# Optimization experiments

Hardware: AMD Instinct MI355X
Metric: run time of the kernel (lower is better)

## Reference

```python
import jax, jax.numpy as jnp
import numpy as np

NUM_CLASSES = 4
IGNORE_INDEX = 0
DELTA_POS = 0.9
DELTA_NEG = 0.1
LAMBDA_ALIGN = 1.0
LAMBDA_SEP = 1.0
EPS = 1e-6
MIN_PIXELS = 1
NORM_EPS = 1e-12  # torch F.normalize default


def setup_inputs() -> dict:
    key = jax.random.key(0)
    k1, k2, k3 = jax.random.split(key, 3)
    B, M, C, D, H, W = 2, 4, 64, 48, 48, 48
    feats = jax.random.normal(k1, (B, M, C, D, H, W), dtype=jnp.float32)
    weights = jax.random.uniform(k2, (B, M, D, H, W), dtype=jnp.float32)
    target = jax.random.randint(k3, (B, 1, D, H, W), 0, NUM_CLASSES, dtype=jnp.int64)
    return {"feats": feats, "weights": weights, "target": target}


def _loss(feats, weights, target):
    B, M, C, D, H, W = feats.shape
    V = D * H * W
    K = NUM_CLASSES
    f = feats.reshape(B, M, C, V)
    w = weights.reshape(B, M, V)
    tgt = target.reshape(B, V)

    # per-class masks [B, K, V]
    onehot = (tgt[:, None, :] == jnp.arange(K)[None, :, None]).astype(f.dtype)
    count = onehot.sum(-1)  # [B, K] pixel counts (independent of m)

    # total weighted mass per (b, m, k) and omega weighting
    tw = jnp.einsum('bmv,bkv->bmk', w, onehot) + EPS          # [B, M, K]
    omega = tw / (count[:, None, :] + EPS)                     # [B, M, K]

    # weighted class means -> prototypes [B, M, K, C]
    num = jnp.einsum('bmcv,bmv,bkv->bmkc', f, w, onehot)
    proto = num / tw[..., None]
    sumsq = jnp.sum(proto * proto, axis=-1)
    norm = jnp.sqrt(jnp.maximum(sumsq, NORM_EPS * NORM_EPS))   # safe sqrt
    proto = proto / jnp.maximum(norm, NORM_EPS)[..., None]

    # validity: enough pixels and not the ignored class
    valid = (count >= MIN_PIXELS) & (jnp.arange(K) != IGNORE_INDEX)[None, :]
    valid = jnp.broadcast_to(valid[:, None, :], (B, M, K))     # [B, M, K]

    # --- align: same class k, modality pairs m < n ---
    sim_a = jnp.einsum('bmkc,bnkc->bmnk', proto, proto)        # [B, M, M, K]
    tri_m = jnp.triu(jnp.ones((M, M), bool), 1)[None, :, :, None]
    pair_a = valid[:, :, None, :] & valid[:, None, :, :] & tri_m
    om_pair = omega[:, :, None, :] * omega[:, None, :, :]
    align_sum = jnp.where(pair_a, om_pair * jax.nn.relu(DELTA_POS - sim_a), 0.0).sum()
    cnt_align = pair_a.sum().astype(f.dtype)

    # --- sep: same modality m, class pairs k1 < k2 ---
    sim_s = jnp.einsum('bmkc,bmlc->bmkl', proto, proto)        # [B, M, K, K]
    tri_k = jnp.triu(jnp.ones((K, K), bool), 1)[None, None, :, :]
    pair_s = valid[:, :, :, None] & valid[:, :, None, :] & tri_k
    sep_sum = jnp.where(pair_s, jax.nn.relu(sim_s - DELTA_NEG), 0.0).sum()
    cnt_sep = pair_s.sum().astype(f.dtype)

    loss_align = align_sum / (cnt_align + EPS)
    loss_sep = sep_sum / (cnt_sep + EPS)
    return LAMBDA_ALIGN * loss_align + LAMBDA_SEP * loss_sep


def reference(feats, weights, target):
    return _loss(feats, weights, target)
```

## Files before the change

### kernel.cpp

```cpp
#include <hip/hip_runtime.h>
#include <math.h>

#define B_ 2
#define M_ 4
#define C_ 64
#define V_ 110592
#define K_ 4
#define EPS_ 1e-6f

#define WS_NUM 0
#define WS_TW  2048
#define WS_CNT 2080
#define WS_TOTAL 2088

__constant__ int PM_[6] = {0,0,0,1,1,2};
__constant__ int PN_[6] = {1,2,3,2,3,3};

__global__ __launch_bounds__(256) void stats_kernel(
    const float* __restrict__ w, const int* __restrict__ tgt,
    float* __restrict__ ws)
{
    const int SA = 27;
    int bm = blockIdx.x / SA;
    int s  = blockIdx.x % SA;
    int b  = bm >> 2;

    const int vec_per = V_ / 4;
    const int chunk   = vec_per / SA;

    const float4* w4 = (const float4*)(w + (size_t)bm * V_);
    const int4*   t4 = (const int4*)(tgt + (size_t)b * V_);

    float tw0=0.f, tw1=0.f, tw2=0.f, tw3=0.f;
    int   c0=0, c1=0, c2=0, c3=0;

    int end = (s + 1) * chunk;
    for (int i = s * chunk + threadIdx.x; i < end; i += 256) {
        float4 wv = w4[i];
        int4   kv = t4[i];
        tw0 += (kv.x==0?wv.x:0.f) + (kv.y==0?wv.y:0.f) + (kv.z==0?wv.z:0.f) + (kv.w==0?wv.w:0.f);
        tw1 += (kv.x==1?wv.x:0.f) + (kv.y==1?wv.y:0.f) + (kv.z==1?wv.z:0.f) + (kv.w==1?wv.w:0.f);
        tw2 += (kv.x==2?wv.x:0.f) + (kv.y==2?wv.y:0.f) + (kv.z==2?wv.z:0.f) + (kv.w==2?wv.w:0.f);
        tw3 += (kv.x==3?wv.x:0.f) + (kv.y==3?wv.y:0.f) + (kv.z==3?wv.z:0.f) + (kv.w==3?wv.w:0.f);
        c0 += (kv.x==0) + (kv.y==0) + (kv.z==0) + (kv.w==0);
        c1 += (kv.x==1) + (kv.y==1) + (kv.z==1) + (kv.w==1);
        c2 += (kv.x==2) + (kv.y==2) + (kv.z==2) + (kv.w==2);
        c3 += (kv.x==3) + (kv.y==3) + (kv.z==3) + (kv.w==3);
    }

    for (int off = 32; off; off >>= 1) {
        tw0 += __shfl_down(tw0, off); tw1 += __shfl_down(tw1, off);
        tw2 += __shfl_down(tw2, off); tw3 += __shfl_down(tw3, off);
        c0  += __shfl_down(c0,  off); c1  += __shfl_down(c1,  off);
        c2  += __shfl_down(c2,  off); c3  += __shfl_down(c3,  off);
    }
    __shared__ float s_tw[4][4];
    __shared__ int   s_c[4][4];
    int wid = threadIdx.x >> 6, lane = threadIdx.x & 63;
    if (lane == 0) {
        s_tw[wid][0]=tw0; s_tw[wid][1]=tw1; s_tw[wid][2]=tw2; s_tw[wid][3]=tw3;
        s_c[wid][0]=c0;   s_c[wid][1]=c1;   s_c[wid][2]=c2;   s_c[wid][3]=c3;
    }
    __syncthreads();
    if (threadIdx.x < 4) {
        int k = threadIdx.x;
        float t = s_tw[0][k] + s_tw[1][k] + s_tw[2][k] + s_tw[3][k];
        atomicAdd(&ws[WS_TW + bm*4 + k], t);
        if ((bm & 3) == 0) {
            int cc = s_c[0][k] + s_c[1][k] + s_c[2][k] + s_c[3][k];
            atomicAdd(&ws[WS_CNT + b*4 + k], (float)cc);
        }
    }
}

__global__ __launch_bounds__(256) void num_kernel(
    const float* __restrict__ f, const float* __restrict__ w,
    const int* __restrict__ tgt, float* __restrict__ ws)
{
    const int S = 4;
    int idx = blockIdx.x;
    int s  = idx & 3;
    int c  = (idx >> 2) & 63;
    int bm = idx >> 8;
    int b  = bm >> 2;

    const int vec_per = V_ / 4;
    const int chunk   = vec_per / S;

    const float4* f4 = (const float4*)(f + ((size_t)bm * C_ + c) * V_);
    const float4* w4 = (const float4*)(w + (size_t)bm * V_);
    const int4*   t4 = (const int4*)(tgt + (size_t)b * V_);

    float a0=0.f, a1=0.f, a2=0.f, a3=0.f;
    int end = (s + 1) * chunk;
    for (int i = s * chunk + threadIdx.x; i < end; i += 256) {
        float4 fv = f4[i];
        float4 wv = w4[i];
        int4   kv = t4[i];
        float p0 = fv.x * wv.x;
        float p1 = fv.y * wv.y;
        float p2 = fv.z * wv.z;
        float p3 = fv.w * wv.w;
        a0 += (kv.x==0?p0:0.f) + (kv.y==0?p1:0.f) + (kv.z==0?p2:0.f) + (kv.w==0?p3:0.f);
        a1 += (kv.x==1?p0:0.f) + (kv.y==1?p1:0.f) + (kv.z==1?p2:0.f) + (kv.w==1?p3:0.f);
        a2 += (kv.x==2?p0:0.f) + (kv.y==2?p1:0.f) + (kv.z==2?p2:0.f) + (kv.w==2?p3:0.f);
        a3 += (kv.x==3?p0:0.f) + (kv.y==3?p1:0.f) + (kv.z==3?p2:0.f) + (kv.w==3?p3:0.f);
    }

    for (int off = 32; off; off >>= 1) {
        a0 += __shfl_down(a0, off); a1 += __shfl_down(a1, off);
        a2 += __shfl_down(a2, off); a3 += __shfl_down(a3, off);
    }
    __shared__ float s_red[4][4];
    int wid = threadIdx.x >> 6, lane = threadIdx.x & 63;
    if (lane == 0) {
        s_red[wid][0]=a0; s_red[wid][1]=a1; s_red[wid][2]=a2; s_red[wid][3]=a3;
    }
    __syncthreads();
    if (threadIdx.x < 4) {
        int k = threadIdx.x;
        float v = s_red[0][k] + s_red[1][k] + s_red[2][k] + s_red[3][k];
        atomicAdd(&ws[WS_NUM + (bm*4 + k)*C_ + c], v);
    }
}

__global__ __launch_bounds__(256) void finalize_kernel(
    const float* __restrict__ ws, float* __restrict__ out)
{
    const float* num = ws + WS_NUM;
    const float* tw  = ws + WS_TW;
    const float* cnt = ws + WS_CNT;

    __shared__ float sp[2048];
    __shared__ float s_scale[32];
    __shared__ float s_om[32];
    __shared__ int   s_valid[32];

    int tid = threadIdx.x;

    for (int i = tid; i < 2048; i += 256) {
        int p = i >> 6;
        sp[i] = num[i] / (tw[p] + EPS_);
    }
    __syncthreads();

    if (tid < 32) {
        float ss = 0.f;
        for (int c = 0; c < 64; ++c) { float v = sp[tid*64 + c]; ss += v*v; }
        float norm = sqrtf(fmaxf(ss, 1e-24f));
        s_scale[tid] = 1.0f / fmaxf(norm, 1e-12f);
        int b = tid >> 4;
        int k = tid & 3;
        float cc = cnt[b*4 + k];
        s_om[tid] = (tw[tid] + EPS_) / (cc + EPS_);
        s_valid[tid] = (cc >= 1.0f) && (k != 0);
    }
    __syncthreads();
    for (int i = tid; i < 2048; i += 256) sp[i] *= s_scale[i >> 6];
    __syncthreads();

    float aS = 0.f, aC = 0.f, sS = 0.f, sC = 0.f;

    if (tid < 48) {
        int b = tid / 24, r = tid % 24;
        int pr = r >> 2, k = r & 3;
        int p1 = (b*4 + PM_[pr])*4 + k;
        int p2 = (b*4 + PN_[pr])*4 + k;
        if (s_valid[p1] && s_valid[p2]) {
            float d = 0.f;
            for (int c = 0; c < 64; ++c) d += sp[p1*64 + c] * sp[p2*64 + c];
            aS = s_om[p1] * s_om[p2] * fmaxf(0.9f - d, 0.f);
            aC = 1.f;
        }
    } else if (tid >= 64 && tid < 112) {
        int t = tid - 64;
        int b = t / 24, r = t % 24;
        int m = r / 6, pr = r % 6;
        int bm = b*4 + m;
        int p1 = bm*4 + PM_[pr];
        int p2 = bm*4 + PN_[pr];
        if (s_valid[p1] && s_valid[p2]) {
            float d = 0.f;
            for (int c = 0; c < 64; ++c) d += sp[p1*64 + c] * sp[p2*64 + c];
            sS = fmaxf(d - 0.1f, 0.f);
            sC = 1.f;
        }
    }

    for (int off = 32; off; off >>= 1) {
        aS += __shfl_down(aS, off); aC += __shfl_down(aC, off);
        sS += __shfl_down(sS, off); sC += __shfl_down(sC, off);
    }
    __shared__ float red[4][4];
    int wid = tid >> 6, lane = tid & 63;
    if (lane == 0) { red[wid][0]=aS; red[wid][1]=aC; red[wid][2]=sS; red[wid][3]=sC; }
    __syncthreads();
    if (tid == 0) {
        float AS=0.f, AC=0.f, SS=0.f, SC=0.f;
        for (int i = 0; i < 4; ++i) { AS+=red[i][0]; AC+=red[i][1]; SS+=red[i][2]; SC+=red[i][3]; }
        out[0] = AS / (AC + EPS_) + SS / (SC + EPS_);
    }
}

extern "C" void kernel_launch(void* const* d_in, const int* in_sizes, int n_in,
                              void* d_out, int out_size, void* d_ws, size_t ws_size,
                              hipStream_t stream)
{
    const float* feats   = (const float*)d_in[0];
    const float* weights = (const float*)d_in[1];
    const int*   target  = (const int*)d_in[2];
    float* out = (float*)d_out;
    float* ws  = (float*)d_ws;

    hipMemsetAsync(d_ws, 0, WS_TOTAL * sizeof(float), stream);
    stats_kernel<<<B_*M_*27, 256, 0, stream>>>(weights, target, ws);
    num_kernel<<<B_*M_*C_*4, 256, 0, stream>>>(feats, weights, target, ws);
    finalize_kernel<<<1, 256, 0, stream>>>(ws, out);
}
```

Baseline: 327.0 us.

## Fuse stats into feature reduction, process two channels per block, drop atomics

Merges the separate weight/count statistics kernel into the main feature-reduction kernel, computed only by channel-0 blocks. Each block now handles two channels so the weight and target loads are shared. Feature loads become nontemporal. Per-split partial sums go to distinct workspace slots that the finalize kernel adds up, which removes the memset and the atomics. The cost is more registers per thread, fewer blocks, and a little extra reduction work in the single-block finalize.

```diff
diff --git a/kernel.cpp b/kernel.cpp
--- a/kernel.cpp
+++ b/kernel.cpp
@@ -5,154 +5,151 @@
 #define M_ 4
 #define C_ 64
 #define V_ 110592
-#define K_ 4
 #define EPS_ 1e-6f
 
-#define WS_NUM 0
-#define WS_TW  2048
-#define WS_CNT 2080
-#define WS_TOTAL 2088
+#define P_NUM 0
+#define P_TW  8192
+#define P_CNT 8320
 
 __constant__ int PM_[6] = {0,0,0,1,1,2};
 __constant__ int PN_[6] = {1,2,3,2,3,3};
 
-__global__ __launch_bounds__(256) void stats_kernel(
-    const float* __restrict__ w, const int* __restrict__ tgt,
-    float* __restrict__ ws)
-{
-    const int SA = 27;
-    int bm = blockIdx.x / SA;
-    int s  = blockIdx.x % SA;
-    int b  = bm >> 2;
-
-    const int vec_per = V_ / 4;
-    const int chunk   = vec_per / SA;
-
-    const float4* w4 = (const float4*)(w + (size_t)bm * V_);
-    const int4*   t4 = (const int4*)(tgt + (size_t)b * V_);
-
-    float tw0=0.f, tw1=0.f, tw2=0.f, tw3=0.f;
-    int   c0=0, c1=0, c2=0, c3=0;
-
-    int end = (s + 1) * chunk;
-    for (int i = s * chunk + threadIdx.x; i < end; i += 256) {
-        float4 wv = w4[i];
-        int4   kv = t4[i];
-        tw0 += (kv.x==0?wv.x:0.f) + (kv.y==0?wv.y:0.f) + (kv.z==0?wv.z:0.f) + (kv.w==0?wv.w:0.f);
-        tw1 += (kv.x==1?wv.x:0.f) + (kv.y==1?wv.y:0.f) + (kv.z==1?wv.z:0.f) + (kv.w==1?wv.w:0.f);
-        tw2 += (kv.x==2?wv.x:0.f) + (kv.y==2?wv.y:0.f) + (kv.z==2?wv.z:0.f) + (kv.w==2?wv.w:0.f);
-        tw3 += (kv.x==3?wv.x:0.f) + (kv.y==3?wv.y:0.f) + (kv.z==3?wv.z:0.f) + (kv.w==3?wv.w:0.f);
-        c0 += (kv.x==0) + (kv.y==0) + (kv.z==0) + (kv.w==0);
-        c1 += (kv.x==1) + (kv.y==1) + (kv.z==1) + (kv.w==1);
-        c2 += (kv.x==2) + (kv.y==2) + (kv.z==2) + (kv.w==2);
-        c3 += (kv.x==3) + (kv.y==3) + (kv.z==3) + (kv.w==3);
-    }
-
-    for (int off = 32; off; off >>= 1) {
-        tw0 += __shfl_down(tw0, off); tw1 += __shfl_down(tw1, off);
-        tw2 += __shfl_down(tw2, off); tw3 += __shfl_down(tw3, off);
-        c0  += __shfl_down(c0,  off); c1  += __shfl_down(c1,  off);
-        c2  += __shfl_down(c2,  off); c3  += __shfl_down(c3,  off);
-    }
-    __shared__ float s_tw[4][4];
-    __shared__ int   s_c[4][4];
-    int wid = threadIdx.x >> 6, lane = threadIdx.x & 63;
-    if (lane == 0) {
-        s_tw[wid][0]=tw0; s_tw[wid][1]=tw1; s_tw[wid][2]=tw2; s_tw[wid][3]=tw3;
-        s_c[wid][0]=c0;   s_c[wid][1]=c1;   s_c[wid][2]=c2;   s_c[wid][3]=c3;
-    }
-    __syncthreads();
-    if (threadIdx.x < 4) {
-        int k = threadIdx.x;
-        float t = s_tw[0][k] + s_tw[1][k] + s_tw[2][k] + s_tw[3][k];
-        atomicAdd(&ws[WS_TW + bm*4 + k], t);
-        if ((bm & 3) == 0) {
-            int cc = s_c[0][k] + s_c[1][k] + s_c[2][k] + s_c[3][k];
-            atomicAdd(&ws[WS_CNT + b*4 + k], (float)cc);
-        }
-    }
-}
-
-__global__ __launch_bounds__(256) void num_kernel(
+typedef float  fvec4 __attribute__((ext_vector_type(4)));
+
+__global__ __launch_bounds__(256) void main_kernel(
     const float* __restrict__ f, const float* __restrict__ w,
     const int* __restrict__ tgt, float* __restrict__ ws)
 {
-    const int S = 4;
     int idx = blockIdx.x;
     int s  = idx & 3;
-    int c  = (idx >> 2) & 63;
-    int bm = idx >> 8;
+    int ch = (idx >> 2) & 31;
+    int bm = idx >> 7;
     int b  = bm >> 2;
-
-    const int vec_per = V_ / 4;
-    const int chunk   = vec_per / S;
-
-    const float4* f4 = (const float4*)(f + ((size_t)bm * C_ + c) * V_);
+    const bool do_stats = (ch == 0);
+
+    const int chunk = (V_ / 4) / 4;
+
+    const fvec4* fa = (const fvec4*)(f + ((size_t)bm * C_ + ch) * V_);
+    const fvec4* fb = (const fvec4*)(f + ((size_t)bm * C_ + ch + 32) * V_);
     const float4* w4 = (const float4*)(w + (size_t)bm * V_);
     const int4*   t4 = (const int4*)(tgt + (size_t)b * V_);
 
-    float a0=0.f, a1=0.f, a2=0.f, a3=0.f;
-    int end = (s + 1) * chunk;
-    for (int i = s * chunk + threadIdx.x; i < end; i += 256) {
-        float4 fv = f4[i];
+    float A[8] = {0,0,0,0,0,0,0,0};
+    float tw[4] = {0,0,0,0};
+    int   cn[4] = {0,0,0,0};
+
+    int beg = s * chunk, end = beg + chunk;
+    for (int i = beg + (int)threadIdx.x; i < end; i += 256) {
+        fvec4  va = __builtin_nontemporal_load(&fa[i]);
+        fvec4  vb = __builtin_nontemporal_load(&fb[i]);
         float4 wv = w4[i];
         int4   kv = t4[i];
-        float p0 = fv.x * wv.x;
-        float p1 = fv.y * wv.y;
-        float p2 = fv.z * wv.z;
-        float p3 = fv.w * wv.w;
-        a0 += (kv.x==0?p0:0.f) + (kv.y==0?p1:0.f) + (kv.z==0?p2:0.f) + (kv.w==0?p3:0.f);
-        a1 += (kv.x==1?p0:0.f) + (kv.y==1?p1:0.f) + (kv.z==1?p2:0.f) + (kv.w==1?p3:0.f);
-        a2 += (kv.x==2?p0:0.f) + (kv.y==2?p1:0.f) + (kv.z==2?p2:0.f) + (kv.w==2?p3:0.f);
-        a3 += (kv.x==3?p0:0.f) + (kv.y==3?p1:0.f) + (kv.z==3?p2:0.f) + (kv.w==3?p3:0.f);
-    }
-
+        float pa0 = va.x * wv.x, pa1 = va.y * wv.y, pa2 = va.z * wv.z, pa3 = va.w * wv.w;
+        float pb0 = vb.x * wv.x, pb1 = vb.y * wv.y, pb2 = vb.z * wv.z, pb3 = vb.w * wv.w;
+        #pragma unroll
+        for (int k = 0; k < 4; ++k) {
+            A[k]     += (kv.x==k?pa0:0.f) + (kv.y==k?pa1:0.f) + (kv.z==k?pa2:0.f) + (kv.w==k?pa3:0.f);
+            A[4 + k] += (kv.x==k?pb0:0.f) + (kv.y==k?pb1:0.f) + (kv.z==k?pb2:0.f) + (kv.w==k?pb3:0.f);
+        }
+        if (do_stats) {
+            #pragma unroll
+            for (int k = 0; k < 4; ++k) {
+                tw[k] += (kv.x==k?wv.x:0.f) + (kv.y==k?wv.y:0.f) + (kv.z==k?wv.z:0.f) + (kv.w==k?wv.w:0.f);
+                cn[k] += (kv.x==k) + (kv.y==k) + (kv.z==k) + (kv.w==k);
+            }
+        }
+    }
+
+    #pragma unroll
     for (int off = 32; off; off >>= 1) {
-        a0 += __shfl_down(a0, off); a1 += __shfl_down(a1, off);
-        a2 += __shfl_down(a2, off); a3 += __shfl_down(a3, off);
-    }
-    __shared__ float s_red[4][4];
+        #pragma unroll
+        for (int j = 0; j < 8; ++j) A[j] += __shfl_down(A[j], off);
+        if (do_stats) {
+            #pragma unroll
+            for (int k = 0; k < 4; ++k) {
+                tw[k] += __shfl_down(tw[k], off);
+                cn[k] += __shfl_down(cn[k], off);
+            }
+        }
+    }
+
+    __shared__ float sA[4][8];
+    __shared__ float sT[4][4];
+    __shared__ int   sC[4][4];
     int wid = threadIdx.x >> 6, lane = threadIdx.x & 63;
     if (lane == 0) {
-        s_red[wid][0]=a0; s_red[wid][1]=a1; s_red[wid][2]=a2; s_red[wid][3]=a3;
-    }
-    __syncthreads();
-    if (threadIdx.x < 4) {
+        #pragma unroll
+        for (int j = 0; j < 8; ++j) sA[wid][j] = A[j];
+        if (do_stats) {
+            #pragma unroll
+            for (int k = 0; k < 4; ++k) { sT[wid][k] = tw[k]; sC[wid][k] = cn[k]; }
+        }
+    }
+    __syncthreads();
+
+    if (threadIdx.x < 8) {
+        int j = threadIdx.x;
+        int k = j & 3;
+        int c = ch + (j >> 2) * 32;
+        float v = sA[0][j] + sA[1][j] + sA[2][j] + sA[3][j];
+        ws[P_NUM + ((bm * C_ + c) * 4 + s) * 4 + k] = v;
+    }
+    if (do_stats && threadIdx.x < 4) {
         int k = threadIdx.x;
-        float v = s_red[0][k] + s_red[1][k] + s_red[2][k] + s_red[3][k];
-        atomicAdd(&ws[WS_NUM + (bm*4 + k)*C_ + c], v);
+        float t = sT[0][k] + sT[1][k] + sT[2][k] + sT[3][k];
+        ws[P_TW + (bm * 4 + s) * 4 + k] = t;
+        if ((bm & 3) == 0) {
+            int cc = sC[0][k] + sC[1][k] + sC[2][k] + sC[3][k];
+            ws[P_CNT + (b * 4 + s) * 4 + k] = (float)cc;
+        }
     }
 }
 
 __global__ __launch_bounds__(256) void finalize_kernel(
     const float* __restrict__ ws, float* __restrict__ out)
 {
-    const float* num = ws + WS_NUM;
-    const float* tw  = ws + WS_TW;
-    const float* cnt = ws + WS_CNT;
-
     __shared__ float sp[2048];
+    __shared__ float s_tw[32];
+    __shared__ float s_cnt[8];
     __shared__ float s_scale[32];
     __shared__ float s_om[32];
     __shared__ int   s_valid[32];
 
     int tid = threadIdx.x;
 
+    if (tid < 32) {
+        int bm = tid >> 2, k = tid & 3;
+        float t = 0.f;
+        #pragma unroll
+        for (int s = 0; s < 4; ++s) t += ws[P_TW + (bm * 4 + s) * 4 + k];
+        s_tw[tid] = t;
+    } else if (tid < 40) {
+        int u = tid - 32, b = u >> 2, k = u & 3;
+        float t = 0.f;
+        #pragma unroll
+        for (int s = 0; s < 4; ++s) t += ws[P_CNT + (b * 4 + s) * 4 + k];
+        s_cnt[u] = t;
+    }
+    __syncthreads();
+
     for (int i = tid; i < 2048; i += 256) {
-        int p = i >> 6;
-        sp[i] = num[i] / (tw[p] + EPS_);
+        int p = i >> 6, c = i & 63;
+        int bm = p >> 2, k = p & 3;
+        float t = 0.f;
+        #pragma unroll
+        for (int s = 0; s < 4; ++s) t += ws[P_NUM + ((bm * C_ + c) * 4 + s) * 4 + k];
+        sp[i] = t / (s_tw[p] + EPS_);
     }
     __syncthreads();
 
     if (tid < 32) {
         float ss = 0.f;
-        for (int c = 0; c < 64; ++c) { float v = sp[tid*64 + c]; ss += v*v; }
+        for (int c = 0; c < 64; ++c) { float v = sp[tid * 64 + c]; ss += v * v; }
         float norm = sqrtf(fmaxf(ss, 1e-24f));
         s_scale[tid] = 1.0f / fmaxf(norm, 1e-12f);
-        int b = tid >> 4;
-        int k = tid & 3;
-        float cc = cnt[b*4 + k];
-        s_om[tid] = (tw[tid] + EPS_) / (cc + EPS_);
+        int b = tid >> 4, k = tid & 3;
+        float cc = s_cnt[b * 4 + k];
+        s_om[tid] = (s_tw[tid] + EPS_) / (cc + EPS_);
         s_valid[tid] = (cc >= 1.0f) && (k != 0);
     }
     __syncthreads();
@@ -164,11 +161,11 @@
     if (tid < 48) {
         int b = tid / 24, r = tid % 24;
         int pr = r >> 2, k = r & 3;
-        int p1 = (b*4 + PM_[pr])*4 + k;
-        int p2 = (b*4 + PN_[pr])*4 + k;
+        int p1 = (b * 4 + PM_[pr]) * 4 + k;
+        int p2 = (b * 4 + PN_[pr]) * 4 + k;
         if (s_valid[p1] && s_valid[p2]) {
             float d = 0.f;
-            for (int c = 0; c < 64; ++c) d += sp[p1*64 + c] * sp[p2*64 + c];
+            for (int c = 0; c < 64; ++c) d += sp[p1 * 64 + c] * sp[p2 * 64 + c];
             aS = s_om[p1] * s_om[p2] * fmaxf(0.9f - d, 0.f);
             aC = 1.f;
         }
@@ -176,17 +173,18 @@
         int t = tid - 64;
         int b = t / 24, r = t % 24;
         int m = r / 6, pr = r % 6;
-        int bm = b*4 + m;
-        int p1 = bm*4 + PM_[pr];
-        int p2 = bm*4 + PN_[pr];
+        int bm = b * 4 + m;
+        int p1 = bm * 4 + PM_[pr];
+        int p2 = bm * 4 + PN_[pr];
         if (s_valid[p1] && s_valid[p2]) {
             float d = 0.f;
-            for (int c = 0; c < 64; ++c) d += sp[p1*64 + c] * sp[p2*64 + c];
+            for (int c = 0; c < 64; ++c) d += sp[p1 * 64 + c] * sp[p2 * 64 + c];
             sS = fmaxf(d - 0.1f, 0.f);
             sC = 1.f;
         }
     }
 
+    #pragma unroll
     for (int off = 32; off; off >>= 1) {
         aS += __shfl_down(aS, off); aC += __shfl_down(aC, off);
         sS += __shfl_down(sS, off); sC += __shfl_down(sC, off);
@@ -197,6 +195,7 @@
     __syncthreads();
     if (tid == 0) {
         float AS=0.f, AC=0.f, SS=0.f, SC=0.f;
+        #pragma unroll
         for (int i = 0; i < 4; ++i) { AS+=red[i][0]; AC+=red[i][1]; SS+=red[i][2]; SC+=red[i][3]; }
         out[0] = AS / (AC + EPS_) + SS / (SC + EPS_);
     }
@@ -212,8 +211,6 @@
     float* out = (float*)d_out;
     float* ws  = (float*)d_ws;
 
-    hipMemsetAsync(d_ws, 0, WS_TOTAL * sizeof(float), stream);
-    stats_kernel<<<B_*M_*27, 256, 0, stream>>>(weights, target, ws);
-    num_kernel<<<B_*M_*C_*4, 256, 0, stream>>>(feats, weights, target, ws);
+    main_kernel<<<B_*M_*32*4, 256, 0, stream>>>(feats, weights, target, ws);
     finalize_kernel<<<1, 256, 0, stream>>>(ws, out);
 }
```

After: 307.4 us. 1.06x faster.
